# Kernel optimization log

Hardware: AMD Instinct MI355X
Metric: run time of the kernel (lower is better)

The kernel has to match this reference:

```python
import jax, jax.numpy as jnp
import numpy as np

HEADS = 16
D_MODEL = 1024
D_K = D_MODEL // HEADS


def setup_inputs() -> dict:
    key = jax.random.key(0)
    ks = jax.random.split(key, 8)
    B, S = 4, 2048
    scale = 1.0 / np.sqrt(D_MODEL)
    return {
        "queries": jax.random.normal(ks[0], (B, S, D_MODEL), dtype=jnp.float32),
        "keys": jax.random.normal(ks[1], (B, S, D_MODEL), dtype=jnp.float32),
        "values": jax.random.normal(ks[2], (B, S, D_MODEL), dtype=jnp.float32),
        # Per-head projection weights, stacked over heads: [H, d_model, d_k]
        "Wq": jax.random.normal(ks[3], (HEADS, D_MODEL, D_K), dtype=jnp.float32) * scale,
        "Wk": jax.random.normal(ks[4], (HEADS, D_MODEL, D_K), dtype=jnp.float32) * scale,
        "Wv": jax.random.normal(ks[5], (HEADS, D_MODEL, D_K), dtype=jnp.float32) * scale,
        "Wout": jax.random.normal(ks[6], (D_MODEL, D_MODEL), dtype=jnp.float32) * scale,
        "bout": jax.random.normal(ks[7], (D_MODEL,), dtype=jnp.float32) * 0.01,
    }


def reference(queries, keys, values, Wq, Wk, Wv, Wout, bout):
    # Per-head linear projections (torch Linear: x @ W.T, here W stored as [H, d_model, d_k])
    q = jnp.einsum("bsd,hdk->bhsk", queries, Wq)   # [B,H,S,d_k]
    k = jnp.einsum("btd,hdk->bhtk", keys, Wk)      # [B,H,T,d_k]
    v = jnp.einsum("btd,hdv->bhtv", values, Wv)    # [B,H,T,d_v]
    scores = jnp.einsum("bhsk,bhtk->bhst", q, k) / jnp.sqrt(jnp.float32(D_K))
    probs = jax.nn.softmax(scores, axis=-1)        # [B,H,S,T]
    wv = jnp.einsum("bhst,bhtv->bhsv", probs, v)   # [B,H,S,d_v]
    # concat heads along last dim: [B,S,H*d_v] == [B,S,d_model]
    B, H, S, Dv = wv.shape
    concat = jnp.transpose(wv, (0, 2, 1, 3)).reshape(B, S, H * Dv)
    return concat @ Wout.T + bout
```

## Files before the change

### kernel.cpp

```cpp
#include <hip/hip_runtime.h>
#include <hip/hip_bf16.h>
#include <stdint.h>

#define DM 1024
#define SZ ((size_t)8192*1024)
#define WSZ ((size_t)1024*1024)

typedef float  f32x2  __attribute__((ext_vector_type(2)));
typedef float  f32x4  __attribute__((ext_vector_type(4)));
typedef float  f32x16 __attribute__((ext_vector_type(16)));
typedef __bf16 bf16x8 __attribute__((ext_vector_type(8)));
typedef __bf16 bf16x2 __attribute__((ext_vector_type(2)));
typedef short  s16x8  __attribute__((ext_vector_type(8)));
typedef unsigned int u32;
typedef unsigned int u32x4 __attribute__((ext_vector_type(4)));

typedef const __attribute__((address_space(1))) void* gas_ptr;
typedef __attribute__((address_space(3))) void* las_ptr;

static __device__ __forceinline__ f32x4 mfma16(s16x8 a, s16x8 b, f32x4 c){
  return __builtin_amdgcn_mfma_f32_16x16x32_bf16(
      __builtin_bit_cast(bf16x8, a), __builtin_bit_cast(bf16x8, b), c, 0, 0, 0);
}
static __device__ __forceinline__ f32x16 mfma32(s16x8 a, s16x8 b, f32x16 c){
  return __builtin_amdgcn_mfma_f32_32x32x16_bf16(
      __builtin_bit_cast(bf16x8, a), __builtin_bit_cast(bf16x8, b), c, 0, 0, 0);
}

static __device__ __forceinline__ u32 pack2(float a, float b){
  bf16x2 v = { (__bf16)a, (__bf16)b };
  return __builtin_bit_cast(u32, v);
}
static __device__ __forceinline__ short f2bf(float f){
  __bf16 v = (__bf16)f;
  return __builtin_bit_cast(short, v);
}

static __device__ __forceinline__ void gload_lds16(void* l, const void* g){
  __builtin_amdgcn_global_load_lds((gas_ptr)g, (las_ptr)l, 16, 0, 0);
}

#define QSCALE 0.1803368801111444f


__global__ void convert_misc(const float* __restrict__ q, const float* __restrict__ k,
                             const float* __restrict__ v, const float* __restrict__ wo,
                             short* __restrict__ ws){
  size_t c = (size_t)blockIdx.x*blockDim.x + threadIdx.x;
  const size_t n8_in = 3*(SZ/8);
  const float* src; short* dst;
  if (c < n8_in){
    int s = (int)(c >> 20);
    size_t off = c*8 - ((size_t)s << 23);
    src = (s==0 ? q : (s==1 ? k : v)) + off;
    dst = ws + c*8;
  } else {
    size_t off = (c - n8_in)*8;
    src = wo + off;
    dst = ws + 6*SZ + 3*WSZ + off;
  }
  float4 a = *(const float4*)src;
  float4 b = *(const float4*)(src + 4);
  uint4 o;
  o.x = pack2(a.x, a.y); o.y = pack2(a.z, a.w);
  o.z = pack2(b.x, b.y); o.w = pack2(b.z, b.w);
  *(uint4*)dst = o;
}

__global__ void convert_wqkv(const float* __restrict__ wq, const float* __restrict__ wk,
                             const float* __restrict__ wv, short* __restrict__ ws){
  __shared__ float tile[64][65];
  int bid = blockIdx.x;
  int sel = bid >> 8;
  int h   = (bid >> 4) & 15;
  int dt  = bid & 15;
  const float* W = sel==0 ? wq : (sel==1 ? wk : wv);
  float sc = sel==0 ? QSCALE : 1.0f;
  short* Bt = ws + 6*SZ + (size_t)sel*WSZ;
  int tid = threadIdx.x;
  int r = tid >> 4, c4 = (tid & 15)*4;
  int d0 = dt*64;
  #pragma unroll
  for (int i=0;i<4;i++){
    int d = r + i*16;
    float4 vv = *(const float4*)&W[(size_t)h*65536 + (size_t)(d0+d)*64 + c4];
    tile[d][c4+0]=vv.x*sc; tile[d][c4+1]=vv.y*sc; tile[d][c4+2]=vv.z*sc; tile[d][c4+3]=vv.w*sc;
  }
  __syncthreads();
  #pragma unroll
  for (int i=0;i<4;i++){
    int kk = r + i*16;
    unsigned int lo = pack2(tile[c4+0][kk], tile[c4+1][kk]);
    unsigned int hi = pack2(tile[c4+2][kk], tile[c4+3][kk]);
    *(uint2*)&Bt[(size_t)(h*64+kk)*1024 + d0 + c4] = make_uint2(lo, hi);
  }
}


static __device__ __forceinline__ void gemm_core_bf16(
    const short* __restrict__ A, const short* __restrict__ Bt,
    int bm, int bn, short* As, short* Bs, f32x4 acc[4][4])
{
  int tid = threadIdx.x;
  int w = tid>>6, lane = tid&63;
  int wm = w>>1, wn = w&1;
  int col = lane&15, kg = lane>>4;
  int rs = w*16 + (lane>>2);
  int ch = lane&3;
  int chs = ch ^ (rs & 3);

  auto stage = [&](int buf, int kt){
    #pragma unroll
    for (int it=0; it<2; ++it){
      int r = rs + it*64;
      gload_lds16(As + buf*4096 + r*32 + ch*8,
                  A + (size_t)(bm*128 + r)*1024 + kt*32 + chs*8);
    }
    #pragma unroll
    for (int it=0; it<2; ++it){
      int r = rs + it*64;
      gload_lds16(Bs + buf*4096 + r*32 + ch*8,
                  Bt + (size_t)(bn*128 + r)*1024 + kt*32 + chs*8);
    }
  };

  const f32x4 fzero = {0.f,0.f,0.f,0.f};
  #pragma unroll
  for (int mf=0; mf<4; ++mf)
    #pragma unroll
    for (int nf=0; nf<4; ++nf)
      acc[mf][nf] = fzero;

  int fbase = col*32 + ((kg ^ (col&3))<<3);

  stage(0, 0);
  int buf = 0;
  for (int kt=0; kt<32; ++kt){
    __syncthreads();
    if (kt < 31) stage(buf^1, kt+1);
    s16x8 af[4], bfr[4];
    #pragma unroll
    for (int mf=0; mf<4; ++mf)
      af[mf] = *(const s16x8*)(As + buf*4096 + (wm*64 + mf*16)*32 + fbase);
    #pragma unroll
    for (int nf=0; nf<4; ++nf)
      bfr[nf] = *(const s16x8*)(Bs + buf*4096 + (wn*64 + nf*16)*32 + fbase);
    #pragma unroll
    for (int mf=0; mf<4; ++mf)
      #pragma unroll
      for (int nf=0; nf<4; ++nf)
        acc[mf][nf] = mfma16(af[mf], bfr[nf], acc[mf][nf]);
    buf ^= 1;
  }
}

__global__ __launch_bounds__(256,2) void gemm_qkv(short* __restrict__ ws){
  __shared__ __align__(16) short As[2*4096];
  __shared__ __align__(16) short Bs[2*4096];
  int bid = blockIdx.x;
  bid = (bid & 7)*192 + (bid >> 3);
  int bm = bid / 24, bnq = bid % 24;
  int sel = bnq >> 3, bn = bnq & 7;
  const short* A  = ws + (size_t)sel*SZ;
  const short* Bt = ws + 6*SZ + (size_t)sel*WSZ;
  f32x4 acc[4][4];
  gemm_core_bf16(A, Bt, bm, bn, As, Bs, acc);

  int tid = threadIdx.x, w = tid>>6, lane = tid&63;
  int wm=w>>1, wn=w&1, col=lane&15, kg=lane>>4;
  if (sel == 0){
    short* O = ws + 3*SZ;
    #pragma unroll
    for (int mf=0; mf<4; ++mf){
      int gr0 = bm*128 + wm*64 + mf*16 + kg*4;
      #pragma unroll
      for (int nf=0; nf<4; ++nf){
        int gc = bn*128 + wn*64 + nf*16 + col;
        #pragma unroll
        for (int r=0; r<4; ++r)
          O[(size_t)(gr0+r)*1024 + gc] = f2bf(acc[mf][nf][r]);
      }
    }
  } else if (sel == 1){
    short* Kt = ws + 4*SZ;
    #pragma unroll
    for (int mf=0; mf<4; ++mf){
      int gr0 = bm*128 + wm*64 + mf*16 + kg*4;
      int b = gr0 >> 11, s0 = gr0 & 2047;
      int ts = s0 >> 5, t0 = s0 & 31;
      #pragma unroll
      for (int nf=0; nf<4; ++nf){
        int gc = bn*128 + wn*64 + nf*16 + col;
        int h = gc >> 6, d = gc & 63;
        size_t base = ((size_t)((b*16+h)*64 + ts))*2048 + (size_t)((d>>3)*32)*8 + (d&7);
        #pragma unroll
        for (int r=0; r<4; ++r)
          Kt[base + (size_t)(t0+r)*8] = f2bf(acc[mf][nf][r]);
      }
    }
  } else {
    short* Vt = ws + 5*SZ;
    #pragma unroll
    for (int mf=0; mf<4; ++mf){
      int gr0 = bm*128 + wm*64 + mf*16 + kg*4;
      int b = gr0 >> 11, s0 = gr0 & 2047;
      int ts = s0 >> 5, c2 = (s0 >> 3) & 3, j0 = s0 & 7;
      #pragma unroll
      for (int nf=0; nf<4; ++nf){
        int gc = bn*128 + wn*64 + nf*16 + col;
        int h = gc >> 6, dv = gc & 63;
        unsigned int lo = pack2(acc[mf][nf][0], acc[mf][nf][1]);
        unsigned int hi = pack2(acc[mf][nf][2], acc[mf][nf][3]);
        size_t addr = ((size_t)((b*16+h)*64 + ts))*2048 + (size_t)(c2*64 + dv)*8 + j0;
        *(uint2*)&Vt[addr] = make_uint2(lo, hi);
      }
    }
  }
}

__global__ __launch_bounds__(256,2) void gemm_out(const short* __restrict__ cc,
                                                  const short* __restrict__ BtO,
                                                  const float* __restrict__ bias,
                                                  float* __restrict__ out){
  __shared__ __align__(16) short As[2*4096];
  __shared__ __align__(16) short Bs[2*4096];
  int bid = blockIdx.x;
  bid = (bid & 7)*64 + (bid >> 3);
  int bm = bid >> 3, bn = bid & 7;
  f32x4 acc[4][4];
  gemm_core_bf16(cc, BtO, bm, bn, As, Bs, acc);

  int tid = threadIdx.x, w=tid>>6, lane=tid&63;
  int wm=w>>1, wn=w&1, col=lane&15, kg=lane>>4;
  #pragma unroll
  for (int nf=0; nf<4; ++nf){
    int gc = bn*128 + wn*64 + nf*16 + col;
    float bb = bias[gc];
    #pragma unroll
    for (int mf=0; mf<4; ++mf){
      int gr0 = bm*128 + wm*64 + mf*16 + kg*4;
      #pragma unroll
      for (int r=0; r<4; ++r)
        out[(size_t)(gr0+r)*1024 + gc] = acc[mf][nf][r] + bb;
    }
  }
}

__global__ __launch_bounds__(256,2) void attn(const short* __restrict__ qp,
                                              const short* __restrict__ kpT,
                                              const short* __restrict__ vTt,
                                              short* __restrict__ cc){
  int bid = blockIdx.x;
  bid = (bid & 7)*64 + (bid >> 3);
  int qb = bid & 7, h = (bid>>3) & 15, b = bid >> 7;
  int bh = b*16 + h;
  int tid = threadIdx.x, w = tid>>6, lane = tid&63;
  int ql = lane & 31, hi = lane >> 5;
  int qbase = qb*256 + w*64;

  const short* qg = qp + ((size_t)(b*2048 + qbase + ql))*1024 + h*64;
  s16x8 qf[2][4];
  #pragma unroll
  for (int qt=0; qt<2; ++qt)
    #pragma unroll
    for (int ks=0; ks<4; ++ks)
      qf[qt][ks] = *(const s16x8*)(qg + qt*32*1024 + ks*16 + hi*8);

  const short* kfb = kpT + (size_t)(bh*64)*2048 + hi*256 + ql*8;
  const short* vfb = vTt + (size_t)(bh*64)*2048 + hi*512 + ql*8;

  const f32x16 z16 = {0.f,0.f,0.f,0.f,0.f,0.f,0.f,0.f,
                      0.f,0.f,0.f,0.f,0.f,0.f,0.f,0.f};
  f32x16 o[2][2] = {{z16, z16}, {z16, z16}};
  float l0 = 0.f, l1 = 0.f;

  auto packP = [&](f32x16& s, s16x8* pb){
    u32 a0 = pack2(s[0], s[1]),  b0 = pack2(s[2], s[3]);
    u32 c0 = pack2(s[4], s[5]),  d0 = pack2(s[6], s[7]);
    asm("v_permlane32_swap_b32 %0, %1" : "+v"(a0), "+v"(c0));
    asm("v_permlane32_swap_b32 %0, %1" : "+v"(b0), "+v"(d0));
    u32x4 t0v = {a0, b0, c0, d0};
    pb[0] = __builtin_bit_cast(s16x8, t0v);
    u32 a1 = pack2(s[8], s[9]),   b1 = pack2(s[10], s[11]);
    u32 c1 = pack2(s[12], s[13]), d1 = pack2(s[14], s[15]);
    asm("v_permlane32_swap_b32 %0, %1" : "+v"(a1), "+v"(c1));
    asm("v_permlane32_swap_b32 %0, %1" : "+v"(b1), "+v"(d1));
    u32x4 t1v = {a1, b1, c1, d1};
    pb[1] = __builtin_bit_cast(s16x8, t1v);
  };

  s16x8 kf[4];
  #pragma unroll
  for (int ks=0; ks<4; ++ks)
    kf[ks] = *(const s16x8*)(kfb + ks*512);

  for (int ts = 0; ts < 64; ++ts){
    const short* vsrc = vfb + (size_t)ts*2048;
    s16x8 vf0 = *(const s16x8*)(vsrc);
    s16x8 vf1 = *(const s16x8*)(vsrc + 256);
    s16x8 vf2 = *(const s16x8*)(vsrc + 1024);
    s16x8 vf3 = *(const s16x8*)(vsrc + 1280);

    f32x16 s0 = z16, s1 = z16;
    __builtin_amdgcn_s_setprio(1);
    #pragma unroll
    for (int ks=0; ks<4; ++ks){
      s0 = mfma32(kf[ks], qf[0][ks], s0);
      s1 = mfma32(kf[ks], qf[1][ks], s1);
    }
    __builtin_amdgcn_s_setprio(0);

    if (ts < 63){
      const short* ksrc = kfb + (size_t)(ts+1)*2048;
      #pragma unroll
      for (int ks=0; ks<4; ++ks)
        kf[ks] = *(const s16x8*)(ksrc + ks*512);
    }

    f32x2 la = {0.f,0.f}, lb = {0.f,0.f};
    #pragma unroll
    for (int i=0;i<16;i+=4){
      s0[i]   = __builtin_amdgcn_exp2f(s0[i]);
      s0[i+1] = __builtin_amdgcn_exp2f(s0[i+1]);
      s0[i+2] = __builtin_amdgcn_exp2f(s0[i+2]);
      s0[i+3] = __builtin_amdgcn_exp2f(s0[i+3]);
      f32x2 pa = {s0[i], s0[i+1]}, pbv = {s0[i+2], s0[i+3]};
      la += pa; lb += pbv;
    }
    l0 += (la[0]+la[1]) + (lb[0]+lb[1]);
    f32x2 lc = {0.f,0.f}, ld = {0.f,0.f};
    #pragma unroll
    for (int i=0;i<16;i+=4){
      s1[i]   = __builtin_amdgcn_exp2f(s1[i]);
      s1[i+1] = __builtin_amdgcn_exp2f(s1[i+1]);
      s1[i+2] = __builtin_amdgcn_exp2f(s1[i+2]);
      s1[i+3] = __builtin_amdgcn_exp2f(s1[i+3]);
      f32x2 pa = {s1[i], s1[i+1]}, pbv = {s1[i+2], s1[i+3]};
      lc += pa; ld += pbv;
    }
    l1 += (lc[0]+lc[1]) + (ld[0]+ld[1]);

    s16x8 pb0[2], pb1[2];
    packP(s0, pb0);
    packP(s1, pb1);

    __builtin_amdgcn_s_setprio(1);
    o[0][0] = mfma32(vf0, pb0[0], o[0][0]);
    o[1][0] = mfma32(vf0, pb1[0], o[1][0]);
    o[0][1] = mfma32(vf1, pb0[0], o[0][1]);
    o[1][1] = mfma32(vf1, pb1[0], o[1][1]);
    o[0][0] = mfma32(vf2, pb0[1], o[0][0]);
    o[1][0] = mfma32(vf2, pb1[1], o[1][0]);
    o[0][1] = mfma32(vf3, pb0[1], o[0][1]);
    o[1][1] = mfma32(vf3, pb1[1], o[1][1]);
    __builtin_amdgcn_s_setprio(0);
  }

  l0 += __shfl_xor(l0, 32);
  l1 += __shfl_xor(l1, 32);
  float rc0 = 1.0f / l0, rc1 = 1.0f / l1;
  #pragma unroll
  for (int qt=0; qt<2; ++qt){
    float rcl = qt ? rc1 : rc0;
    short* og = cc + ((size_t)(b*2048 + qbase + qt*32 + ql))*1024 + h*64;
    #pragma unroll
    for (int dvt=0; dvt<2; ++dvt){
      #pragma unroll
      for (int s=0; s<4; ++s){
        int dv0 = dvt*32 + s*8 + hi*4;
        uint2 wd;
        wd.x = pack2(o[qt][dvt][s*4+0]*rcl, o[qt][dvt][s*4+1]*rcl);
        wd.y = pack2(o[qt][dvt][s*4+2]*rcl, o[qt][dvt][s*4+3]*rcl);
        *(uint2*)&og[dv0] = wd;
      }
    }
  }
}


extern "C" void kernel_launch(void* const* d_in, const int* in_sizes, int n_in,
                              void* d_out, int out_size, void* d_ws, size_t ws_size,
                              hipStream_t stream){
  const float* q  = (const float*)d_in[0];
  const float* k  = (const float*)d_in[1];
  const float* v  = (const float*)d_in[2];
  const float* wq = (const float*)d_in[3];
  const float* wk = (const float*)d_in[4];
  const float* wv = (const float*)d_in[5];
  const float* wo = (const float*)d_in[6];
  const float* bo = (const float*)d_in[7];
  short* ws = (short*)d_ws;
  float* out = (float*)d_out;

  size_t needed = (6*SZ + 4*WSZ)*sizeof(short);
  if (ws_size < needed) return;

  convert_misc<<<12800, 256, 0, stream>>>(q, k, v, wo, ws);
  convert_wqkv<<<768, 256, 0, stream>>>(wq, wk, wv, ws);
  gemm_qkv<<<1536, 256, 0, stream>>>(ws);
  attn<<<512, 256, 0, stream>>>(ws + 3*SZ, ws + 4*SZ, ws + 5*SZ, ws);
  gemm_out<<<512, 256, 0, stream>>>(ws, ws + 6*SZ + 3*WSZ, bo, out);
}
```

Baseline: 198.3 us.

## Fuse fp32-to-bf16 activation conversion into QKV GEMM A-tile loads

```diff
diff --git a/kernel.cpp b/kernel.cpp
--- a/kernel.cpp
+++ b/kernel.cpp
@@ -43,28 +43,14 @@
 #define QSCALE 0.1803368801111444f
 
 
-__global__ void convert_misc(const float* __restrict__ q, const float* __restrict__ k,
-                             const float* __restrict__ v, const float* __restrict__ wo,
-                             short* __restrict__ ws){
-  size_t c = (size_t)blockIdx.x*blockDim.x + threadIdx.x;
-  const size_t n8_in = 3*(SZ/8);
-  const float* src; short* dst;
-  if (c < n8_in){
-    int s = (int)(c >> 20);
-    size_t off = c*8 - ((size_t)s << 23);
-    src = (s==0 ? q : (s==1 ? k : v)) + off;
-    dst = ws + c*8;
-  } else {
-    size_t off = (c - n8_in)*8;
-    src = wo + off;
-    dst = ws + 6*SZ + 3*WSZ + off;
-  }
-  float4 a = *(const float4*)src;
-  float4 b = *(const float4*)(src + 4);
+__global__ void convert_wo(const float* __restrict__ wo, short* __restrict__ dst){
+  size_t i = ((size_t)blockIdx.x*blockDim.x + threadIdx.x)*8;
+  float4 a = *(const float4*)(wo + i);
+  float4 b = *(const float4*)(wo + i + 4);
   uint4 o;
   o.x = pack2(a.x, a.y); o.y = pack2(a.z, a.w);
   o.z = pack2(b.x, b.y); o.w = pack2(b.z, b.w);
-  *(uint4*)dst = o;
+  *(uint4*)(dst + i) = o;
 }
 
 __global__ void convert_wqkv(const float* __restrict__ wq, const float* __restrict__ wk,
@@ -154,20 +140,83 @@
   }
 }
 
-__global__ __launch_bounds__(256,2) void gemm_qkv(short* __restrict__ ws){
-  __shared__ __align__(16) short As[2*4096];
+__global__ __launch_bounds__(256,2) void gemm_qkv(const float* __restrict__ q,
+                                                  const float* __restrict__ k,
+                                                  const float* __restrict__ v,
+                                                  short* __restrict__ ws){
+  __shared__ __align__(16) float Af[2*4096];
   __shared__ __align__(16) short Bs[2*4096];
-  int bid = blockIdx.x;
-  bid = (bid & 7)*192 + (bid >> 3);
-  int bm = bid / 24, bnq = bid % 24;
-  int sel = bnq >> 3, bn = bnq & 7;
-  const short* A  = ws + (size_t)sel*SZ;
+  int o = blockIdx.x;
+  int x = o & 7, j = o >> 3;
+  int bn = j & 7;
+  int pid = x*24 + (j >> 3);
+  int bm = pid / 3, sel = pid % 3;
+  const float* A  = sel==0 ? q : (sel==1 ? k : v);
   const short* Bt = ws + 6*SZ + (size_t)sel*WSZ;
+
+  int tid = threadIdx.x;
+  int w = tid>>6, lane = tid&63;
+  int wm = w>>1, wn = w&1;
+  int col = lane&15, kg = lane>>4;
+
+  int rs = w*16 + (lane>>2);
+  int ch = lane&3;
+  int chs = ch ^ (rs & 3);
+  const short* bg = Bt + (size_t)(bn*128 + rs)*1024 + chs*8;
+
+  int rl8 = lane>>3, c8 = lane&7;
+  int csrc = c8 ^ rl8;
+  const float* ag = A + (size_t)(bm*128 + w*32 + rl8)*1024 + csrc*4;
+
+  auto stage = [&](int buf, int kt){
+    #pragma unroll
+    for (int i=0; i<4; ++i)
+      gload_lds16(Af + buf*4096 + w*1024 + i*256 + lane*4,
+                  ag + (size_t)i*8192 + kt*32);
+    gload_lds16(Bs + buf*4096 + rs*32 + ch*8, bg + kt*32);
+    gload_lds16(Bs + buf*4096 + (rs+64)*32 + ch*8, bg + (size_t)64*1024 + kt*32);
+  };
+
   f32x4 acc[4][4];
-  gemm_core_bf16(A, Bt, bm, bn, As, Bs, acc);
-
-  int tid = threadIdx.x, w = tid>>6, lane = tid&63;
-  int wm=w>>1, wn=w&1, col=lane&15, kg=lane>>4;
+  const f32x4 fzero = {0.f,0.f,0.f,0.f};
+  #pragma unroll
+  for (int mf=0; mf<4; ++mf)
+    #pragma unroll
+    for (int nf=0; nf<4; ++nf)
+      acc[mf][nf] = fzero;
+
+  int fbase = col*32 + ((kg ^ (col&3))<<3);
+  int cx = col & 7;
+  int aoff0 = ((2*kg)   ^ cx) * 4;
+  int aoff1 = ((2*kg+1) ^ cx) * 4;
+
+  stage(0, 0);
+  int buf = 0;
+  for (int kt=0; kt<32; ++kt){
+    __syncthreads();
+    if (kt < 31) stage(buf^1, kt+1);
+    s16x8 af[4], bfr[4];
+    #pragma unroll
+    for (int mf=0; mf<4; ++mf){
+      const float* arow = Af + buf*4096 + (wm*64 + mf*16 + col)*32;
+      f32x4 a0 = *(const f32x4*)(arow + aoff0);
+      f32x4 a1 = *(const f32x4*)(arow + aoff1);
+      u32x4 w4;
+      w4[0] = pack2(a0[0], a0[1]); w4[1] = pack2(a0[2], a0[3]);
+      w4[2] = pack2(a1[0], a1[1]); w4[3] = pack2(a1[2], a1[3]);
+      af[mf] = __builtin_bit_cast(s16x8, w4);
+    }
+    #pragma unroll
+    for (int nf=0; nf<4; ++nf)
+      bfr[nf] = *(const s16x8*)(Bs + buf*4096 + (wn*64 + nf*16)*32 + fbase);
+    #pragma unroll
+    for (int mf=0; mf<4; ++mf)
+      #pragma unroll
+      for (int nf=0; nf<4; ++nf)
+        acc[mf][nf] = mfma16(af[mf], bfr[nf], acc[mf][nf]);
+    buf ^= 1;
+  }
+
   if (sel == 0){
     short* O = ws + 3*SZ;
     #pragma unroll
@@ -395,9 +444,9 @@
   size_t needed = (6*SZ + 4*WSZ)*sizeof(short);
   if (ws_size < needed) return;
 
-  convert_misc<<<12800, 256, 0, stream>>>(q, k, v, wo, ws);
+  convert_wo<<<512, 256, 0, stream>>>(wo, ws + 6*SZ + 3*WSZ);
   convert_wqkv<<<768, 256, 0, stream>>>(wq, wk, wv, ws);
-  gemm_qkv<<<1536, 256, 0, stream>>>(ws);
+  gemm_qkv<<<1536, 256, 0, stream>>>(q, k, v, ws);
   attn<<<512, 256, 0, stream>>>(ws + 3*SZ, ws + 4*SZ, ws + 5*SZ, ws);
   gemm_out<<<512, 256, 0, stream>>>(ws, ws + 6*SZ + 3*WSZ, bo, out);
 }
```

New measurement: 199.4 us. No clear change (+0.5%).
